# Optimization experiments

Measured on AMD Instinct MI355X. Metric: run time of the kernel, lower is better.

The kernel has to match this reference:

```python
import jax, jax.numpy as jnp
import numpy as np

IN_F = 4096
OUT_F = 4096
PACKED_IN = IN_F // 16  # 16 ternary values per int32 (2 bits each)
TOKENS = 8192


def _pack(vals_int32):
    # vals_int32: [out, packed_in, 16] with entries in {0,1,2}
    shifts = (jnp.arange(16, dtype=jnp.int32) * 2)
    return jnp.sum(vals_int32 << shifts, axis=-1).astype(jnp.int32)


def _unpack_weight(packed, scale, in_features):
    # packed: [out, packed_in] int32 -> fp32 weight [out, in_features]
    shifts = (jnp.arange(16, dtype=jnp.int32) * 2)
    vals = (packed[:, :, None] >> shifts) & 3           # [out, packed_in, 16]
    w = vals.reshape(packed.shape[0], -1)[:, :in_features]
    return (w.astype(jnp.float32) - 1.0) * scale


def setup_inputs() -> dict:
    key = jax.random.key(0)
    k1, k2 = jax.random.split(key)
    x = jax.random.normal(k1, (TOKENS, IN_F), dtype=jnp.float32)
    # mapped ternary values in {0,1,2} (i.e. w_ternary + 1), packed 2-bit
    mapped = jax.random.randint(k2, (OUT_F, PACKED_IN, 16), 0, 3, dtype=jnp.int32)
    packed_weight = _pack(mapped)
    scale = jnp.float32(0.02)
    return {"x": x, "packed_weight": packed_weight, "scale": scale}


def reference(x, packed_weight, scale):
    # dequantize ternary weight
    w = _unpack_weight(packed_weight, scale, IN_F)      # [out, in]
    # abs-max activation scaling along the last dim
    x_scale = jnp.clip(jnp.max(jnp.abs(x), axis=-1, keepdims=True), 1e-5, None)
    x_scaled = x / x_scale
    out = jnp.einsum('ti,oi->to', x_scaled, w)          # F.linear (no bias)
    return out * x_scale
```

## Files before the change

### kernel.cpp

```cpp
#include <hip/hip_runtime.h>
#include <math.h>

typedef __attribute__((ext_vector_type(4)))  int   i32x4;
typedef __attribute__((ext_vector_type(16))) int   i32x16;
typedef __attribute__((ext_vector_type(4)))  float f32x4;

namespace {
constexpr int IN_F   = 4096;
constexpr int OUT_F  = 4096;
constexpr int TOKENS = 8192;
constexpr int PACKED = IN_F / 16;

constexpr int BM   = 256;
constexpr int BN   = 128;
constexpr int BK   = 128;
constexpr int NTHR = 256;
constexpr size_t XQ_BYTES = (size_t)TOKENS * IN_F;
}

__global__ __launch_bounds__(256)
void rowquant(const float* __restrict__ X, signed char* __restrict__ XQ,
              float* __restrict__ XS) {
  const int row  = blockIdx.x * 4 + (threadIdx.x >> 6);
  const int lane = threadIdx.x & 63;
  const float* xr = X + (size_t)row * IN_F;

  f32x4 v[16];
  float m = 0.f;
#pragma unroll
  for (int c = 0; c < 16; ++c) {
    v[c] = *(const f32x4*)(xr + c * 256 + lane * 4);
    m = fmaxf(m, fmaxf(fmaxf(fabsf(v[c].x), fabsf(v[c].y)),
                       fmaxf(fabsf(v[c].z), fabsf(v[c].w))));
  }
#pragma unroll
  for (int off = 32; off; off >>= 1) m = fmaxf(m, __shfl_xor(m, off, 64));
  m = fmaxf(m, 1e-5f);
  const float r = 127.f / m;

#pragma unroll
  for (int c = 0; c < 16; ++c) {
    int q0 = (int)rintf(v[c].x * r);
    int q1 = (int)rintf(v[c].y * r);
    int q2 = (int)rintf(v[c].z * r);
    int q3 = (int)rintf(v[c].w * r);
    unsigned d = (q0 & 255) | ((q1 & 255) << 8) | ((q2 & 255) << 16) | ((q3 & 255) << 24);
    *(unsigned*)(XQ + (size_t)row * IN_F + c * 256 + lane * 4) = d;
  }
  if (lane == 0) XS[row] = m;
}

__device__ __forceinline__ i32x4 unpack16(unsigned w) {
  i32x4 r;
#pragma unroll
  for (int g = 0; g < 4; ++g) {
    unsigned t = (w >> (8 * g)) & 0xFFu;
    unsigned s = (t | (t << 6) | (t << 12) | (t << 18)) & 0x03030303u;
    r[g] = (int)((((s | 0x80808080u) - 0x01010101u) ^ 0x80808080u));
  }
  return r;
}

__global__ __launch_bounds__(NTHR, 2)
void gemm_i8(const signed char* __restrict__ XQ, const unsigned* __restrict__ PW,
             const float* __restrict__ XS, const float* __restrict__ SC,
             float* __restrict__ OUT) {
  __shared__ signed char lA[BM * BK];

  const int tid  = threadIdx.x;
  const int lane = tid & 63;
  const int w    = tid >> 6;
  const int wm   = w >> 1;
  const int wn   = w & 1;
  const int l31  = lane & 31;
  const int h    = lane >> 5;

  const int m0 = blockIdx.y * BM;
  const int n0 = blockIdx.x * BN;

  i32x16 acc[4][2];
#pragma unroll
  for (int mf = 0; mf < 4; ++mf)
#pragma unroll
    for (int nf = 0; nf < 2; ++nf)
      acc[mf][nf] = (i32x16)(0);

  const unsigned* pb0 = PW + (size_t)(n0 + wn * 64 + 0 * 32 + l31) * PACKED;
  const unsigned* pb1 = PW + (size_t)(n0 + wn * 64 + 1 * 32 + l31) * PACKED;

  for (int kt = 0; kt < IN_F / BK; ++kt) {
#pragma unroll
    for (int cc = 0; cc < 2; ++cc) {
      const int c = w * 2 + cc;
#pragma unroll
      for (int rb = 0; rb < 4; ++rb) {
        const signed char* src =
            XQ + (size_t)(m0 + rb * 64 + lane) * IN_F + kt * BK + c * 16;
        signed char* dst = lA + c * 4096 + rb * 1024;
        __builtin_amdgcn_global_load_lds(
            (const __attribute__((address_space(1))) void*)src,
            (__attribute__((address_space(3))) void*)dst, 16, 0, 0);
      }
    }

    unsigned bw0[4], bw1[4];
#pragma unroll
    for (int ks = 0; ks < 4; ++ks) {
      bw0[ks] = pb0[kt * 8 + ks * 2 + h];
      bw1[ks] = pb1[kt * 8 + ks * 2 + h];
    }

    __syncthreads();

#pragma unroll
    for (int ks = 0; ks < 4; ++ks) {
      i32x4 bfr0 = unpack16(bw0[ks]);
      i32x4 bfr1 = unpack16(bw1[ks]);
      i32x4 afr[4];
#pragma unroll
      for (int mf = 0; mf < 4; ++mf)
        afr[mf] = *(const i32x4*)(lA + (ks * 2 + h) * 4096 +
                                  (wm * 128 + mf * 32 + l31) * 16);
#pragma unroll
      for (int mf = 0; mf < 4; ++mf) {
        acc[mf][0] = __builtin_amdgcn_mfma_i32_32x32x32_i8(afr[mf], bfr0, acc[mf][0], 0, 0, 0);
        acc[mf][1] = __builtin_amdgcn_mfma_i32_32x32x32_i8(afr[mf], bfr1, acc[mf][1], 0, 0, 0);
      }
    }
    __syncthreads();
  }

  const float sc = SC[0] / 127.f;
#pragma unroll
  for (int mf = 0; mf < 4; ++mf) {
    float fs[16];
#pragma unroll
    for (int r = 0; r < 16; ++r) {
      const int mm = m0 + wm * 128 + mf * 32 + 4 * h + (r & 3) + 8 * (r >> 2);
      fs[r] = sc * XS[mm];
    }
#pragma unroll
    for (int nf = 0; nf < 2; ++nf) {
      const int ncol = n0 + wn * 64 + nf * 32 + l31;
#pragma unroll
      for (int r = 0; r < 16; ++r) {
        const int mm = m0 + wm * 128 + mf * 32 + 4 * h + (r & 3) + 8 * (r >> 2);
        OUT[(size_t)mm * OUT_F + ncol] = (float)acc[mf][nf][r] * fs[r];
      }
    }
  }
}

extern "C" void kernel_launch(void* const* d_in, const int* in_sizes, int n_in,
                              void* d_out, int out_size, void* d_ws, size_t ws_size,
                              hipStream_t stream) {
  const float*    x  = (const float*)d_in[0];
  const unsigned* pw = (const unsigned*)d_in[1];
  const float*    sc = (const float*)d_in[2];
  float*          out = (float*)d_out;

  signed char* xq = (signed char*)d_ws;
  float*       xs = (float*)((char*)d_ws + XQ_BYTES);

  rowquant<<<dim3(TOKENS / 4), dim3(256), 0, stream>>>(x, xq, xs);
  dim3 grid(OUT_F / BN, TOKENS / BM);
  gemm_i8<<<grid, dim3(NTHR), 0, stream>>>(xq, pw, xs, sc, out);
}
```

Measured before the change: 490.1 us.

## Pre-unpack ternary weights, double-buffer A tiles, and remap blocks per XCD

Adds a separate kernel that expands the packed 2-bit weights into an int8 fragment-major buffer, so the GEMM loads ready MFMA B fragments instead of unpacking them in the inner loop. The GEMM now double-buffers the A tile in LDS and prefetches B registers one K-tile ahead, using explicit vmcnt waits and barriers to overlap loads with MFMA work. Blocks are remapped so each XCD works on a contiguous group of N tiles, aiming at better L2 reuse. rowquant is also reshaped to one row per block. In exchange it needs extra workspace and an extra launch, reads 4x more B bytes, and uses twice the LDS, which may lower occupancy. It falls back to the old path when the workspace is too small.

```diff
diff --git a/kernel.cpp b/kernel.cpp
--- a/kernel.cpp
+++ b/kernel.cpp
@@ -15,39 +15,13 @@
 constexpr int BN   = 128;
 constexpr int BK   = 128;
 constexpr int NTHR = 256;
+constexpr int NT   = IN_F / BK;
+
 constexpr size_t XQ_BYTES = (size_t)TOKENS * IN_F;
-}
-
-__global__ __launch_bounds__(256)
-void rowquant(const float* __restrict__ X, signed char* __restrict__ XQ,
-              float* __restrict__ XS) {
-  const int row  = blockIdx.x * 4 + (threadIdx.x >> 6);
-  const int lane = threadIdx.x & 63;
-  const float* xr = X + (size_t)row * IN_F;
-
-  f32x4 v[16];
-  float m = 0.f;
-#pragma unroll
-  for (int c = 0; c < 16; ++c) {
-    v[c] = *(const f32x4*)(xr + c * 256 + lane * 4);
-    m = fmaxf(m, fmaxf(fmaxf(fabsf(v[c].x), fabsf(v[c].y)),
-                       fmaxf(fabsf(v[c].z), fabsf(v[c].w))));
-  }
-#pragma unroll
-  for (int off = 32; off; off >>= 1) m = fmaxf(m, __shfl_xor(m, off, 64));
-  m = fmaxf(m, 1e-5f);
-  const float r = 127.f / m;
-
-#pragma unroll
-  for (int c = 0; c < 16; ++c) {
-    int q0 = (int)rintf(v[c].x * r);
-    int q1 = (int)rintf(v[c].y * r);
-    int q2 = (int)rintf(v[c].z * r);
-    int q3 = (int)rintf(v[c].w * r);
-    unsigned d = (q0 & 255) | ((q1 & 255) << 8) | ((q2 & 255) << 16) | ((q3 & 255) << 24);
-    *(unsigned*)(XQ + (size_t)row * IN_F + c * 256 + lane * 4) = d;
-  }
-  if (lane == 0) XS[row] = m;
+constexpr size_t XS_BYTES = (size_t)TOKENS * 4;
+constexpr size_t BQ_OFF   = XQ_BYTES + XS_BYTES;
+constexpr size_t BQ_BYTES = (size_t)PACKED * OUT_F * 16;
+constexpr size_t WS_NEED  = BQ_OFF + BQ_BYTES;
 }
 
 __device__ __forceinline__ i32x4 unpack16(unsigned w) {
@@ -61,10 +35,181 @@
   return r;
 }
 
+__global__ __launch_bounds__(256)
+void rowquant(const float* __restrict__ X, signed char* __restrict__ XQ,
+              float* __restrict__ XS) {
+  __shared__ float smax[4];
+  const int row = blockIdx.x;
+  const int t   = threadIdx.x;
+  const float* xr = X + (size_t)row * IN_F + t * 16;
+
+  f32x4 v[4];
+  float m = 0.f;
+#pragma unroll
+  for (int j = 0; j < 4; ++j) {
+    v[j] = *(const f32x4*)(xr + j * 4);
+    m = fmaxf(m, fmaxf(fmaxf(fabsf(v[j].x), fabsf(v[j].y)),
+                       fmaxf(fabsf(v[j].z), fabsf(v[j].w))));
+  }
+#pragma unroll
+  for (int off = 32; off; off >>= 1) m = fmaxf(m, __shfl_xor(m, off, 64));
+  if ((t & 63) == 0) smax[t >> 6] = m;
+  __syncthreads();
+  m = fmaxf(fmaxf(smax[0], smax[1]), fmaxf(smax[2], smax[3]));
+  m = fmaxf(m, 1e-5f);
+  const float r = 127.f / m;
+
+  i32x4 d;
+#pragma unroll
+  for (int j = 0; j < 4; ++j) {
+    int q0 = (int)rintf(v[j].x * r);
+    int q1 = (int)rintf(v[j].y * r);
+    int q2 = (int)rintf(v[j].z * r);
+    int q3 = (int)rintf(v[j].w * r);
+    d[j] = (q0 & 255) | ((q1 & 255) << 8) | ((q2 & 255) << 16) | ((q3 & 255) << 24);
+  }
+  *(i32x4*)(XQ + (size_t)row * IN_F + t * 16) = d;
+  if (t == 0) XS[row] = m;
+}
+
+__global__ __launch_bounds__(256)
+void unpackB(const unsigned* __restrict__ PW, signed char* __restrict__ BQ) {
+  const int g = blockIdx.x * 256 + threadIdx.x;
+  const int c = g >> 12;
+  const int n = g & 4095;
+  i32x4 u = unpack16(PW[(size_t)n * PACKED + c]);
+  *(i32x4*)(BQ + ((size_t)c * OUT_F + n) * 16) = u;
+}
+
+#define STAGE_A(BUF, KT)                                                        \
+  {                                                                             \
+    _Pragma("unroll")                                                           \
+    for (int cc = 0; cc < 2; ++cc) {                                            \
+      const int c_ = w * 2 + cc;                                                \
+      _Pragma("unroll")                                                         \
+      for (int rb = 0; rb < 4; ++rb) {                                          \
+        const signed char* src =                                                \
+            XQ + (size_t)(m0 + rb * 64 + lane) * IN_F + (KT) * BK + c_ * 16;    \
+        signed char* dst = lA + (BUF) * 32768 + c_ * 4096 + rb * 1024;          \
+        __builtin_amdgcn_global_load_lds(                                       \
+            (const __attribute__((address_space(1))) void*)src,                 \
+            (__attribute__((address_space(3))) void*)dst, 16, 0, 0);            \
+      }                                                                         \
+    }                                                                           \
+  }
+
+#define LOAD_B(B, KT)                                                           \
+  {                                                                             \
+    _Pragma("unroll")                                                           \
+    for (int nf = 0; nf < 2; ++nf) {                                            \
+      _Pragma("unroll")                                                         \
+      for (int ks = 0; ks < 4; ++ks)                                            \
+        B[nf][ks] = *(const i32x4*)(BQ +                                        \
+            ((size_t)((KT) * 8 + ks * 2 + h) * OUT_F + nrow[nf]) * 16);         \
+      }                                                                         \
+  }
+
+#define COMPUTE_TILE(BUFOFF, B)                                                 \
+  {                                                                             \
+    _Pragma("unroll")                                                           \
+    for (int ks = 0; ks < 4; ++ks) {                                            \
+      i32x4 afr[4];                                                             \
+      _Pragma("unroll")                                                         \
+      for (int mf = 0; mf < 4; ++mf)                                            \
+        afr[mf] = *(const i32x4*)(lA + (BUFOFF) + (ks * 2 + h) * 4096 +         \
+                                  (wm * 128 + mf * 32 + l31) * 16);             \
+      _Pragma("unroll")                                                         \
+      for (int mf = 0; mf < 4; ++mf) {                                          \
+        acc[mf][0] = __builtin_amdgcn_mfma_i32_32x32x32_i8(afr[mf], B[0][ks],   \
+                                                           acc[mf][0], 0, 0, 0);\
+        acc[mf][1] = __builtin_amdgcn_mfma_i32_32x32x32_i8(afr[mf], B[1][ks],   \
+                                                           acc[mf][1], 0, 0, 0);\
+      }                                                                         \
+    }                                                                           \
+  }
+
 __global__ __launch_bounds__(NTHR, 2)
-void gemm_i8(const signed char* __restrict__ XQ, const unsigned* __restrict__ PW,
+void gemm_i8(const signed char* __restrict__ XQ, const signed char* __restrict__ BQ,
              const float* __restrict__ XS, const float* __restrict__ SC,
              float* __restrict__ OUT) {
+  __shared__ signed char lA[2 * 32768];
+
+  const int tid  = threadIdx.x;
+  const int lane = tid & 63;
+  const int w    = tid >> 6;
+  const int wm   = w >> 1;
+  const int wn   = w & 1;
+  const int l31  = lane & 31;
+  const int h    = lane >> 5;
+
+  const int orig = blockIdx.y * gridDim.x + blockIdx.x;
+  const int xcd  = orig & 7;
+  const int idx  = orig >> 3;
+  const int m0   = (idx >> 2) * BM;
+  const int n0   = (xcd * 4 + (idx & 3)) * BN;
+
+  const int nrow[2] = { n0 + wn * 64 + 0 * 32 + l31,
+                        n0 + wn * 64 + 1 * 32 + l31 };
+
+  i32x16 acc[4][2];
+#pragma unroll
+  for (int mf = 0; mf < 4; ++mf)
+#pragma unroll
+    for (int nf = 0; nf < 2; ++nf)
+      acc[mf][nf] = (i32x16)(0);
+
+  i32x4 Ba[2][4], Bb[2][4];
+
+  STAGE_A(0, 0);
+  LOAD_B(Ba, 0);
+
+  for (int kt = 0; kt < NT; kt += 2) {
+    STAGE_A(1, kt + 1);
+    LOAD_B(Bb, kt + 1);
+    asm volatile("s_waitcnt vmcnt(16)" ::: "memory");
+    __builtin_amdgcn_s_barrier();
+    COMPUTE_TILE(0, Ba);
+    asm volatile("" ::: "memory");
+    __builtin_amdgcn_s_barrier();
+
+    if (kt + 2 < NT) {
+      STAGE_A(0, kt + 2);
+      LOAD_B(Ba, kt + 2);
+      asm volatile("s_waitcnt vmcnt(16)" ::: "memory");
+    } else {
+      asm volatile("s_waitcnt vmcnt(0)" ::: "memory");
+    }
+    __builtin_amdgcn_s_barrier();
+    COMPUTE_TILE(32768, Bb);
+    asm volatile("" ::: "memory");
+    __builtin_amdgcn_s_barrier();
+  }
+
+  const float sc = SC[0] / 127.f;
+#pragma unroll
+  for (int mf = 0; mf < 4; ++mf) {
+    float fs[16];
+#pragma unroll
+    for (int r = 0; r < 16; ++r) {
+      const int mm = m0 + wm * 128 + mf * 32 + 4 * h + (r & 3) + 8 * (r >> 2);
+      fs[r] = sc * XS[mm];
+    }
+#pragma unroll
+    for (int nf = 0; nf < 2; ++nf) {
+      const int ncol = n0 + wn * 64 + nf * 32 + l31;
+#pragma unroll
+      for (int r = 0; r < 16; ++r) {
+        const int mm = m0 + wm * 128 + mf * 32 + 4 * h + (r & 3) + 8 * (r >> 2);
+        OUT[(size_t)mm * OUT_F + ncol] = (float)acc[mf][nf][r] * fs[r];
+      }
+    }
+  }
+}
+
+__global__ __launch_bounds__(NTHR, 2)
+void gemm_i8_pw(const signed char* __restrict__ XQ, const unsigned* __restrict__ PW,
+                const float* __restrict__ XS, const float* __restrict__ SC,
+                float* __restrict__ OUT) {
   __shared__ signed char lA[BM * BK];
 
   const int tid  = threadIdx.x;
@@ -162,7 +307,14 @@
   signed char* xq = (signed char*)d_ws;
   float*       xs = (float*)((char*)d_ws + XQ_BYTES);
 
-  rowquant<<<dim3(TOKENS / 4), dim3(256), 0, stream>>>(x, xq, xs);
+  rowquant<<<dim3(TOKENS), dim3(256), 0, stream>>>(x, xq, xs);
+
   dim3 grid(OUT_F / BN, TOKENS / BM);
-  gemm_i8<<<grid, dim3(NTHR), 0, stream>>>(xq, pw, xs, sc, out);
-}
+  if (ws_size >= WS_NEED) {
+    signed char* bq = (signed char*)d_ws + BQ_OFF;
+    unpackB<<<dim3(OUT_F * PACKED / 256), dim3(256), 0, stream>>>(pw, bq);
+    gemm_i8<<<grid, dim3(NTHR), 0, stream>>>(xq, bq, xs, sc, out);
+  } else {
+    gemm_i8_pw<<<grid, dim3(NTHR), 0, stream>>>(xq, pw, xs, sc, out);
+  }
+}
```

After: 419.7 us. -14.4%, faster.
